# Kernel optimization log

Measured on AMD Instinct MI355X. Metric: run time of the kernel, lower is better.

Reference implementation:

```python
import jax, jax.numpy as jnp
import numpy as np

# static config (matches init_kwargs and a standard 4-level FPN for ~800px input)
SPATIAL_SHAPES = ((100, 100), (50, 50), (25, 25), (13, 13))  # (H_l, W_l)
B, C, H, L, P = 2, 256, 8, 4, 4
DFFN = 2048
DH = C // H
LQ = sum(h * w for h, w in SPATIAL_SHAPES)  # 13294


def layer_norm(x, g, b, eps=1e-5):
    m = jnp.mean(x, -1, keepdims=True)
    v = jnp.mean((x - m) ** 2, -1, keepdims=True)
    return (x - m) * jax.lax.rsqrt(v + eps) * g + b


def ms_deform_sample(value, loc, attn):
    # value [B,Lv,H,DH], loc [B,Lq,H,L,P,2] in [0,1], attn [B,Lq,H,L,P]
    value = jnp.transpose(value, (0, 2, 1, 3))  # [B,H,Lv,DH]
    lq = loc.shape[1]
    out = jnp.zeros((B, H, lq, DH), value.dtype)
    start = 0
    for l, (Hl, Wl) in enumerate(SPATIAL_SHAPES):
        v = jax.lax.dynamic_slice_in_dim(value, start, Hl * Wl, axis=2)  # [B,H,N_l,DH]
        # grid_sample(align_corners=False) coords: x = loc_x*W - 0.5
        gx = jnp.transpose(loc[:, :, :, l, :, 0], (0, 2, 1, 3)) * Wl - 0.5  # [B,H,Lq,P]
        gy = jnp.transpose(loc[:, :, :, l, :, 1], (0, 2, 1, 3)) * Hl - 0.5
        aw = jnp.transpose(attn[:, :, :, l, :], (0, 2, 1, 3))  # [B,H,Lq,P]
        x0 = jnp.floor(gx)
        y0 = jnp.floor(gy)
        for dx in (0.0, 1.0):
            for dy in (0.0, 1.0):
                xi = x0 + dx
                yi = y0 + dy
                w = (1.0 - jnp.abs(gx - xi)) * (1.0 - jnp.abs(gy - yi))
                valid = (xi >= 0) & (xi < Wl) & (yi >= 0) & (yi < Hl)
                idx = (jnp.clip(yi, 0, Hl - 1) * Wl + jnp.clip(xi, 0, Wl - 1)).astype(jnp.int32)
                g = jnp.take_along_axis(v, idx.reshape(B, H, -1)[..., None], axis=2)  # [B,H,Lq*P,DH]
                ww = (w * aw * valid.astype(w.dtype))[..., None]  # [B,H,Lq,P,1]
                out = out + jnp.sum(g.reshape(B, H, lq, P, DH) * ww, axis=3)
        start += Hl * Wl
    return jnp.transpose(out, (0, 2, 1, 3)).reshape(B, lq, C)


def setup_inputs() -> dict:
    key = jax.random.key(0)
    ks = jax.random.split(key, 16)
    s = 0.02
    return {
        "src": jax.random.normal(ks[0], (B, LQ, C), jnp.float32),
        "pos": jax.random.normal(ks[1], (B, LQ, C), jnp.float32),
        "reference_points": jax.random.uniform(ks[2], (B, LQ, L, 2), jnp.float32),
        "w_value": jax.random.normal(ks[3], (C, C), jnp.float32) * s,
        "b_value": jnp.zeros((C,), jnp.float32),
        "w_off": jax.random.normal(ks[4], (C, H * L * P * 2), jnp.float32) * s,
        "b_off": jax.random.normal(ks[5], (H * L * P * 2,), jnp.float32) * s,
        "w_attn": jax.random.normal(ks[6], (C, H * L * P), jnp.float32) * s,
        "b_attn": jnp.zeros((H * L * P,), jnp.float32),
        "w_out": jax.random.normal(ks[7], (C, C), jnp.float32) * s,
        "b_out": jnp.zeros((C,), jnp.float32),
        "ln1_g": jnp.ones((C,), jnp.float32),
        "ln1_b": jnp.zeros((C,), jnp.float32),
        "w_ffn1": jax.random.normal(ks[8], (C, DFFN), jnp.float32) * s,
        "b_ffn1": jnp.zeros((DFFN,), jnp.float32),
        "w_ffn2": jax.random.normal(ks[9], (DFFN, C), jnp.float32) * s,
        "b_ffn2": jnp.zeros((C,), jnp.float32),
        "ln2_g": jnp.ones((C,), jnp.float32),
        "ln2_b": jnp.zeros((C,), jnp.float32),
    }


def reference(src, pos, reference_points, w_value, b_value, w_off, b_off, w_attn, b_attn,
              w_out, b_out, ln1_g, ln1_b, w_ffn1, b_ffn1, w_ffn2, b_ffn2, ln2_g, ln2_b):
    # DeformableTransformerEncoderLayer.forward (eval mode, no dropout)
    q = src + pos  # with_pos_embed
    lq = q.shape[1]
    value = (src @ w_value + b_value).reshape(B, -1, H, DH)
    off = (q @ w_off + b_off).reshape(B, lq, H, L, P, 2)
    attn = (q @ w_attn + b_attn).reshape(B, lq, H, L * P)
    attn = jax.nn.softmax(attn, axis=-1).reshape(B, lq, H, L, P)
    # offset_normalizer = (W_l, H_l)
    norm = jnp.array([[w, h] for h, w in SPATIAL_SHAPES], dtype=src.dtype)
    loc = reference_points[:, :, None, :, None, :] + off / norm[None, None, None, :, None, :]
    src2 = ms_deform_sample(value, loc, attn) @ w_out + b_out
    x = layer_norm(src + src2, ln1_g, ln1_b)
    ff = jax.nn.relu(x @ w_ffn1 + b_ffn1) @ w_ffn2 + b_ffn2
    return layer_norm(x + ff, ln2_g, ln2_b)
```

## Files before the change

kernel.cpp:

```cpp
#include <hip/hip_runtime.h>

#define LQN   13294
#define NBAT  2
#define MROWS (NBAT * LQN)
#define CCH   256
#define NHEAD 8
#define DHEAD 32
#define NLVL  4
#define NPT   4
#define DFF   2048

typedef short short8 __attribute__((ext_vector_type(8)));
typedef float f32x4 __attribute__((ext_vector_type(4)));
typedef unsigned short u16;
typedef u16 u16x4 __attribute__((ext_vector_type(4)));

__device__ __forceinline__ u16 f2bf(float f) {
  unsigned int u = __builtin_bit_cast(unsigned int, f);
  u += 0x7fffu + ((u >> 16) & 1u);
  return (u16)(u >> 16);
}
__device__ __forceinline__ float bf2f(u16 s) {
  unsigned int u = ((unsigned int)s) << 16;
  return __builtin_bit_cast(float, u);
}
__device__ __forceinline__ void async16(const void* g, void* l) {
  __builtin_amdgcn_global_load_lds(
      (const __attribute__((address_space(1))) void*)g,
      (__attribute__((address_space(3))) void*)l, 16, 0, 0);
}

template<int OUT_MODE>
__global__ __launch_bounds__(256, 2)
void gemm_bf16(const u16* __restrict__ A, const u16* __restrict__ BT,
               const float* __restrict__ bias, void* __restrict__ Cout,
               int M, int N, int K)
{
  __shared__ u16 As[2][128 * 64];
  __shared__ u16 Bs[2][128 * 64];
  const int t    = threadIdx.x;
  const int lane = t & 63;
  const int wid  = t >> 6;
  const int wm   = wid >> 1, wn = wid & 1;
  const int bm   = blockIdx.x, bn = blockIdx.y;
  const int l15  = lane & 15;
  const int kq   = lane >> 4;

  f32x4 acc[4][4];
#pragma unroll
  for (int m = 0; m < 4; ++m)
#pragma unroll
    for (int n = 0; n < 4; ++n) acc[m][n] = (f32x4)0.0f;

  auto stage = [&](int buf, int kt) {
#pragma unroll
    for (int i = 0; i < 4; ++i) {
      const int c   = i * 256 + t;
      const int row = c >> 3;
      const int kg  = (c & 7) ^ (row & 7);
      int ar = bm * 128 + row; ar = ar < M ? ar : M - 1;
      async16(&A[(size_t)ar * K + kt + kg * 8], &As[buf][c * 8]);
      const int br = bn * 128 + row;
      async16(&BT[(size_t)br * K + kt + kg * 8], &Bs[buf][c * 8]);
    }
  };

  stage(0, 0);
  __syncthreads();
  int cur = 0;

  for (int kt = 0; kt < K; kt += 64) {
    if (kt + 64 < K) stage(cur ^ 1, kt + 64);

#pragma unroll
    for (int kk = 0; kk < 2; ++kk) {
      short8 af[4], bfr[4];
#pragma unroll
      for (int m = 0; m < 4; ++m) {
        const int row = wm * 64 + m * 16 + l15;
        const int xb  = (kk * 64 + kq * 16) ^ ((row & 7) << 4);
        af[m] = *(const short8*)((const char*)&As[cur][0] + row * 128 + xb);
      }
#pragma unroll
      for (int n = 0; n < 4; ++n) {
        const int col = wn * 64 + n * 16 + l15;
        const int xb  = (kk * 64 + kq * 16) ^ ((col & 7) << 4);
        bfr[n] = *(const short8*)((const char*)&Bs[cur][0] + col * 128 + xb);
      }
#pragma unroll
      for (int m = 0; m < 4; ++m)
#pragma unroll
        for (int n = 0; n < 4; ++n)
          acc[m][n] = __builtin_amdgcn_mfma_f32_16x16x32_bf16(af[m], bfr[n], acc[m][n], 0, 0, 0);
    }

    __syncthreads();
    cur ^= 1;
  }

  const int crow0 = bm * 128 + wm * 64;
  const int ccol0 = bn * 128 + wn * 64;
#pragma unroll
  for (int n = 0; n < 4; ++n) {
    int col = ccol0 + n * 16 + l15;
    float bv = bias[col];
#pragma unroll
    for (int m = 0; m < 4; ++m) {
      int rbase = crow0 + m * 16 + kq * 4;
#pragma unroll
      for (int j = 0; j < 4; ++j) {
        int row = rbase + j;
        if (row < M) {
          float v = acc[m][n][j] + bv;
          if constexpr (OUT_MODE == 0) {
            ((float*)Cout)[(size_t)row * N + col] = v;
          } else {
            if constexpr (OUT_MODE == 2) v = fmaxf(v, 0.0f);
            ((u16*)Cout)[(size_t)row * N + col] = f2bf(v);
          }
        }
      }
    }
  }
}

__global__ __launch_bounds__(512, 2)
void ffn_fused(const u16* __restrict__ x_bf, const u16* __restrict__ W1T,
               const u16* __restrict__ W2T, const float* __restrict__ b1,
               const float* __restrict__ b2, float* __restrict__ out)
{
  extern __shared__ char smem[];
  u16* w1s = (u16*)(smem);
  u16* w2s = (u16*)(smem + 65536);
  char* ps = (char*)(smem + 131072);

  const int t    = threadIdx.x;
  const int lane = t & 63;
  const int wid  = t >> 6;
  const int l15  = lane & 15;
  const int kq   = lane >> 4;
  const int bm   = blockIdx.x;
  const int pwm  = wid >> 1, pwn = wid & 1;
  const int wm   = wid >> 2, wn = wid & 3;

  short8 xr[2][8];
#pragma unroll
  for (int m = 0; m < 2; ++m) {
    int ar = bm * 128 + pwm * 32 + m * 16 + l15;
    ar = ar < MROWS ? ar : MROWS - 1;
    const char* xb = (const char*)x_bf + (size_t)ar * 512 + kq * 16;
#pragma unroll
    for (int ks = 0; ks < 8; ++ks)
      xr[m][ks] = *(const short8*)(xb + ks * 64);
  }

  auto stage = [&](int buf, int it) {
#pragma unroll
    for (int i = 0; i < 4; ++i) {
      const int c  = i * 512 + t;
      const int r1 = c >> 5;
      const int k1 = ((c & 31) ^ (r1 & 7)) * 8;
      async16(&W1T[(size_t)(it * 64 + r1) * 256 + k1], &w1s[buf * 16384 + c * 8]);
      const int r2 = c >> 3;
      const int k2 = ((c & 7) ^ (r2 & 7)) * 8;
      async16(&W2T[(size_t)r2 * 2048 + it * 64 + k2], &w2s[buf * 16384 + c * 8]);
    }
  };

  f32x4 acc[4][4];
#pragma unroll
  for (int m = 0; m < 4; ++m)
#pragma unroll
    for (int n = 0; n < 4; ++n) acc[m][n] = (f32x4)0.0f;

  stage(0, 0);
  __syncthreads();

  for (int it = 0; it < 32; ++it) {
    const int cur = it & 1;
    if (it < 31) stage(cur ^ 1, it + 1);

    f32x4 p[2][2];
#pragma unroll
    for (int m = 0; m < 2; ++m)
#pragma unroll
      for (int n = 0; n < 2; ++n) p[m][n] = (f32x4)0.0f;

#pragma unroll
    for (int ks = 0; ks < 8; ++ks) {
      short8 bfr[2];
#pragma unroll
      for (int n = 0; n < 2; ++n) {
        const int wrow = pwn * 32 + n * 16 + l15;
        const int xb   = (ks * 64 + kq * 16) ^ ((wrow & 7) << 4);
        bfr[n] = *(const short8*)((const char*)&w1s[cur * 16384] + wrow * 512 + xb);
      }
#pragma unroll
      for (int m = 0; m < 2; ++m)
#pragma unroll
        for (int n = 0; n < 2; ++n)
          p[m][n] = __builtin_amdgcn_mfma_f32_16x16x32_bf16(xr[m][ks], bfr[n], p[m][n], 0, 0, 0);
    }

#pragma unroll
    for (int n = 0; n < 2; ++n) {
      const int col = pwn * 32 + n * 16 + l15;
      const float bv = b1[it * 64 + col];
      const int chnk = col >> 3;
      const int sub  = (col & 7) * 2;
#pragma unroll
      for (int m = 0; m < 2; ++m)
#pragma unroll
        for (int j = 0; j < 4; ++j) {
          const int prow = pwm * 32 + m * 16 + kq * 4 + j;
          const float v = fmaxf(p[m][n][j] + bv, 0.0f);
          *(u16*)(ps + prow * 160 + ((chnk ^ ((prow >> 2) & 3)) << 4) + sub) = f2bf(v);
        }
    }
    __syncthreads();

#pragma unroll
    for (int kk = 0; kk < 2; ++kk) {
      short8 paf[4], bfr[4];
#pragma unroll
      for (int m = 0; m < 4; ++m) {
        const int arow = wm * 64 + m * 16 + l15;
        const int c    = kk * 4 + kq;
        paf[m] = *(const short8*)(ps + arow * 160 + ((c ^ ((arow >> 2) & 3)) << 4));
      }
#pragma unroll
      for (int n = 0; n < 4; ++n) {
        const int brow = wn * 64 + n * 16 + l15;
        const int xb   = ((kk * 4 + kq) ^ (brow & 7)) * 16;
        bfr[n] = *(const short8*)((const char*)&w2s[cur * 16384] + brow * 128 + xb);
      }
#pragma unroll
      for (int m = 0; m < 4; ++m)
#pragma unroll
        for (int n = 0; n < 4; ++n)
          acc[m][n] = __builtin_amdgcn_mfma_f32_16x16x32_bf16(paf[m], bfr[n], acc[m][n], 0, 0, 0);
    }
    __syncthreads();
  }

  const int crow0 = bm * 128 + wm * 64;
#pragma unroll
  for (int n = 0; n < 4; ++n) {
    const int col = wn * 64 + n * 16 + l15;
    const float bv = b2[col];
#pragma unroll
    for (int m = 0; m < 4; ++m) {
      const int rbase = crow0 + m * 16 + kq * 4;
#pragma unroll
      for (int j = 0; j < 4; ++j) {
        const int row = rbase + j;
        if (row < MROWS) out[(size_t)row * 256 + col] = acc[m][n][j] + bv;
      }
    }
  }
}

__global__ __launch_bounds__(256)
void sampler_kernel(const float* __restrict__ offattn,
                    const float* __restrict__ refp,
                    const u16*  __restrict__ value,
                    u16*        __restrict__ src2)
{
  __shared__ float2 sWI[2][8][65];

  const int t   = threadIdx.x;
  const int r2  = t >> 7;
  const int g   = t & 127;
  const int row = blockIdx.x * 2 + r2;
  const int b   = row / LQN;

  {
    const int h   = g >> 4;
    const int p16 = g & 15;
    const int l   = p16 >> 2;

    const float* oa = offattn + (size_t)row * 384;

    float logit = oa[256 + h * 16 + p16];
    float mx = logit;
#pragma unroll
    for (int o = 1; o < 16; o <<= 1) mx = fmaxf(mx, __shfl_xor(mx, o, 64));
    float e = __expf(logit - mx);
    float s = e;
#pragma unroll
    for (int o = 1; o < 16; o <<= 1) s += __shfl_xor(s, o, 64);
    const float aw = e / s;

    const int Wl = (l == 0) ? 100 : (l == 1) ? 50 : (l == 2) ? 25 : 13;
    const int Hl = Wl;
    const int st = (l == 0) ? 0 : (l == 1) ? 10000 : (l == 2) ? 12500 : 13125;

    const float ox = oa[(h * 16 + p16) * 2 + 0];
    const float oy = oa[(h * 16 + p16) * 2 + 1];
    const float rx = refp[(size_t)row * 8 + l * 2 + 0] * (float)Wl - 0.5f;
    const float ry = refp[(size_t)row * 8 + l * 2 + 1] * (float)Hl - 0.5f;
    const float gx = rx + ox;
    const float gy = ry + oy;
    const float x0f = floorf(gx), y0f = floorf(gy);
    const int   x0 = (int)x0f, y0 = (int)y0f;
    const float fx = gx - x0f, fy = gy - y0f;

#pragma unroll
    for (int c = 0; c < 4; ++c) {
      const int dx = c & 1, dy = c >> 1;
      const int xi = x0 + dx, yi = y0 + dy;
      const float wx = dx ? fx : 1.0f - fx;
      const float wy = dy ? fy : 1.0f - fy;
      const bool valid = (xi >= 0) && (xi < Wl) && (yi >= 0) && (yi < Hl);
      const int xc = min(max(xi, 0), Wl - 1);
      const int yc = min(max(yi, 0), Hl - 1);
      const int idx = st + yc * Wl + xc;
      const float w = wx * wy * aw * (valid ? 1.0f : 0.0f);
      sWI[r2][h][p16 * 4 + c] = make_float2(w, __builtin_bit_cast(float, idx));
    }
  }
  __syncthreads();

  {
    const int h  = g >> 4;
    const int c2 = g & 15;
    const char* vbase = (const char*)value + (size_t)b * LQN * 512 + h * 64 + c2 * 4;
    const float2* wi = sWI[r2][h];

    float acc0 = 0.f, acc1 = 0.f;
#pragma unroll 16
    for (int e = 0; e < 64; ++e) {
      const float2 p = wi[e];
      const float w  = p.x;
      const int  idx = __builtin_bit_cast(int, p.y);
      const unsigned u = *(const unsigned*)(vbase + (size_t)idx * 512);
      const float f0 = __builtin_bit_cast(float, u << 16);
      const float f1 = __builtin_bit_cast(float, u & 0xffff0000u);
      acc0 += f0 * w;
      acc1 += f1 * w;
    }
    const unsigned o = (unsigned)f2bf(acc0) | ((unsigned)f2bf(acc1) << 16);
    *(unsigned*)&src2[(size_t)row * 256 + h * 32 + c2 * 2] = o;
  }
}

template<int WRITE_BF>
__global__ __launch_bounds__(256)
void ln_kernel(const float* __restrict__ Xa, const float* __restrict__ Xb,
               const float* __restrict__ gam, const float* __restrict__ bet,
               float* __restrict__ Yf, u16* __restrict__ Ybf)
{
  const int wid = threadIdx.x >> 6, lane = threadIdx.x & 63;
  const int row = blockIdx.x * 4 + wid;
  const f32x4 va = ((const f32x4*)(Xa + (size_t)row * 256))[lane];
  const f32x4 vb = ((const f32x4*)(Xb + (size_t)row * 256))[lane];
  f32x4 v = va + vb;
  float s1 = v[0] + v[1] + v[2] + v[3];
  float s2 = v[0] * v[0] + v[1] * v[1] + v[2] * v[2] + v[3] * v[3];
#pragma unroll
  for (int off = 32; off; off >>= 1) {
    s1 += __shfl_xor(s1, off, 64);
    s2 += __shfl_xor(s2, off, 64);
  }
  const float mean = s1 * (1.0f / 256.0f);
  const float var  = s2 * (1.0f / 256.0f) - mean * mean;
  const float rstd = rsqrtf(var + 1e-5f);
  const f32x4 gv = ((const f32x4*)gam)[lane];
  const f32x4 bv = ((const f32x4*)bet)[lane];
  f32x4 y;
#pragma unroll
  for (int j = 0; j < 4; ++j) y[j] = (v[j] - mean) * rstd * gv[j] + bv[j];
  ((f32x4*)(Yf + (size_t)row * 256))[lane] = y;
  if constexpr (WRITE_BF) {
    u16x4 o;
#pragma unroll
    for (int j = 0; j < 4; ++j) o[j] = f2bf(y[j]);
    ((u16x4*)(Ybf + (size_t)row * 256))[lane] = o;
  }
}

__global__ __launch_bounds__(256)
void prep_qsrc(const float* __restrict__ src, const float* __restrict__ pos,
               u16* __restrict__ src_bf, u16* __restrict__ q_bf)
{
  const size_t i = (size_t)blockIdx.x * 256 + threadIdx.x;
  const f32x4 s = ((const f32x4*)src)[i];
  const f32x4 p = ((const f32x4*)pos)[i];
  u16x4 sb, qb;
#pragma unroll
  for (int j = 0; j < 4; ++j) { sb[j] = f2bf(s[j]); qb[j] = f2bf(s[j] + p[j]); }
  ((u16x4*)src_bf)[i] = sb;
  ((u16x4*)q_bf)[i]   = qb;
}

__global__ __launch_bounds__(256)
void transpose_cast(const float* __restrict__ W, u16* __restrict__ WT, int K, int N)
{
  const int i = blockIdx.x * 256 + threadIdx.x;
  if (i >= K * N) return;
  const int k = i / N, n = i - k * N;
  WT[(size_t)n * K + k] = f2bf(W[i]);
}

__global__ __launch_bounds__(256)
void concat_bias(const float* __restrict__ b_off, const float* __restrict__ b_attn,
                 float* __restrict__ out)
{
  const int i = blockIdx.x * 256 + threadIdx.x;
  if (i < 256) out[i] = b_off[i];
  else if (i < 384) out[i] = b_attn[i - 256];
}

extern "C" void kernel_launch(void* const* d_in, const int* in_sizes, int n_in,
                              void* d_out, int out_size, void* d_ws, size_t ws_size,
                              hipStream_t stream)
{
  const float* src     = (const float*)d_in[0];
  const float* pos     = (const float*)d_in[1];
  const float* refp    = (const float*)d_in[2];
  const float* w_value = (const float*)d_in[3];
  const float* b_value = (const float*)d_in[4];
  const float* w_off   = (const float*)d_in[5];
  const float* b_off   = (const float*)d_in[6];
  const float* w_attn  = (const float*)d_in[7];
  const float* b_attn  = (const float*)d_in[8];
  const float* w_out   = (const float*)d_in[9];
  const float* b_out   = (const float*)d_in[10];
  const float* ln1_g   = (const float*)d_in[11];
  const float* ln1_b   = (const float*)d_in[12];
  const float* w_ffn1  = (const float*)d_in[13];
  const float* b_ffn1  = (const float*)d_in[14];
  const float* w_ffn2  = (const float*)d_in[15];
  const float* b_ffn2  = (const float*)d_in[16];
  const float* ln2_g   = (const float*)d_in[17];
  const float* ln2_b   = (const float*)d_in[18];

  char* ws = (char*)d_ws;
  size_t off = 0;
  auto alloc = [&](size_t bytes) { void* p = ws + off; off += (bytes + 255) & ~(size_t)255; return p; };

  u16*   src_bf   = (u16*)  alloc((size_t)MROWS * 256 * 2);
  u16*   q_bf     = (u16*)  alloc((size_t)MROWS * 256 * 2);
  float* offattn  = (float*)alloc((size_t)MROWS * 384 * 4);
  u16*   value_bf = (u16*)  alloc((size_t)MROWS * 256 * 2);
  u16*   src2_bf  = (u16*)  alloc((size_t)MROWS * 256 * 2);
  float* x_f32    = (float*)alloc((size_t)MROWS * 256 * 4);
  u16*   WT_val   = (u16*)  alloc(256 * 256 * 2);
  u16*   WT_oa    = (u16*)  alloc(384 * 256 * 2);
  u16*   WT_out   = (u16*)  alloc(256 * 256 * 2);
  u16*   WT_f1    = (u16*)  alloc(2048 * 256 * 2);
  u16*   WT_f2    = (u16*)  alloc((size_t)256 * 2048 * 2);
  float* bias_oa  = (float*)alloc(384 * 4);

  float* src2p = offattn;
  u16*   x_bf  = q_bf;
  float* ff    = (float*)value_bf;

  transpose_cast<<<256, 256, 0, stream>>>(w_value, WT_val, 256, 256);
  transpose_cast<<<256, 256, 0, stream>>>(w_off, WT_oa, 256, 256);
  transpose_cast<<<128, 256, 0, stream>>>(w_attn, WT_oa + 256 * 256, 256, 128);
  transpose_cast<<<256, 256, 0, stream>>>(w_out, WT_out, 256, 256);
  transpose_cast<<<2048, 256, 0, stream>>>(w_ffn1, WT_f1, 256, 2048);
  transpose_cast<<<2048, 256, 0, stream>>>(w_ffn2, WT_f2, 2048, 256);
  concat_bias<<<2, 256, 0, stream>>>(b_off, b_attn, bias_oa);

  prep_qsrc<<<6647, 256, 0, stream>>>(src, pos, src_bf, q_bf);

  gemm_bf16<1><<<dim3(208, 2), 256, 0, stream>>>(src_bf, WT_val, b_value, value_bf, MROWS, 256, 256);
  gemm_bf16<0><<<dim3(208, 3), 256, 0, stream>>>(q_bf, WT_oa, bias_oa, offattn, MROWS, 384, 256);

  sampler_kernel<<<MROWS / 2, 256, 0, stream>>>(offattn, refp, value_bf, src2_bf);

  gemm_bf16<0><<<dim3(208, 2), 256, 0, stream>>>(src2_bf, WT_out, b_out, src2p, MROWS, 256, 256);

  ln_kernel<1><<<6647, 256, 0, stream>>>(src, src2p, ln1_g, ln1_b, x_f32, x_bf);

  static bool attr_set = false;
  if (!attr_set) {
    hipFuncSetAttribute((const void*)ffn_fused,
                        hipFuncAttributeMaxDynamicSharedMemorySize, 151552);
    attr_set = true;
  }
  ffn_fused<<<208, 512, 151552, stream>>>(x_bf, WT_f1, WT_f2, b_ffn1, b_ffn2, ff);

  ln_kernel<0><<<6647, 256, 0, stream>>>(x_f32, ff, ln2_g, ln2_b, (float*)d_out, nullptr);
}
```

Before: 252.3 us.

## Merge weight prep and value/offset GEMMs into single launches; widen sampler loads

```diff
diff --git a/kernel.cpp b/kernel.cpp
--- a/kernel.cpp
+++ b/kernel.cpp
@@ -112,12 +112,105 @@
         int row = rbase + j;
         if (row < M) {
           float v = acc[m][n][j] + bv;
-          if constexpr (OUT_MODE == 0) {
-            ((float*)Cout)[(size_t)row * N + col] = v;
-          } else {
-            if constexpr (OUT_MODE == 2) v = fmaxf(v, 0.0f);
-            ((u16*)Cout)[(size_t)row * N + col] = f2bf(v);
-          }
+          if constexpr (OUT_MODE == 0) ((float*)Cout)[(size_t)row * N + col] = v;
+          else                         ((u16*)Cout)[(size_t)row * N + col] = f2bf(v);
+        }
+      }
+    }
+  }
+}
+
+__global__ __launch_bounds__(256, 2)
+void gemm_dual(const u16* __restrict__ A0, const u16* __restrict__ BT0,
+               const float* __restrict__ bias0, u16* __restrict__ C0,
+               const u16* __restrict__ A1, const u16* __restrict__ BT1,
+               const float* __restrict__ bias1, float* __restrict__ C1)
+{
+  __shared__ u16 As[2][128 * 64];
+  __shared__ u16 Bs[2][128 * 64];
+  const int t    = threadIdx.x;
+  const int lane = t & 63;
+  const int wid  = t >> 6;
+  const int wm   = wid >> 1, wn = wid & 1;
+  const int bm   = blockIdx.x;
+  const int bnG  = blockIdx.y;
+  const bool first = bnG < 2;
+  const u16* A    = first ? A0 : A1;
+  const u16* BT   = first ? BT0 : BT1;
+  const float* bias = first ? bias0 : bias1;
+  const int  N    = first ? 256 : 384;
+  const int  bn   = first ? bnG : bnG - 2;
+  const int l15  = lane & 15;
+  const int kq   = lane >> 4;
+
+  f32x4 acc[4][4];
+#pragma unroll
+  for (int m = 0; m < 4; ++m)
+#pragma unroll
+    for (int n = 0; n < 4; ++n) acc[m][n] = (f32x4)0.0f;
+
+  auto stage = [&](int buf, int kt) {
+#pragma unroll
+    for (int i = 0; i < 4; ++i) {
+      const int c   = i * 256 + t;
+      const int row = c >> 3;
+      const int kg  = (c & 7) ^ (row & 7);
+      int ar = bm * 128 + row; ar = ar < MROWS ? ar : MROWS - 1;
+      async16(&A[(size_t)ar * 256 + kt + kg * 8], &As[buf][c * 8]);
+      const int br = bn * 128 + row;
+      async16(&BT[(size_t)br * 256 + kt + kg * 8], &Bs[buf][c * 8]);
+    }
+  };
+
+  stage(0, 0);
+  __syncthreads();
+  int cur = 0;
+
+  for (int kt = 0; kt < 256; kt += 64) {
+    if (kt + 64 < 256) stage(cur ^ 1, kt + 64);
+
+#pragma unroll
+    for (int kk = 0; kk < 2; ++kk) {
+      short8 af[4], bfr[4];
+#pragma unroll
+      for (int m = 0; m < 4; ++m) {
+        const int row = wm * 64 + m * 16 + l15;
+        const int xb  = (kk * 64 + kq * 16) ^ ((row & 7) << 4);
+        af[m] = *(const short8*)((const char*)&As[cur][0] + row * 128 + xb);
+      }
+#pragma unroll
+      for (int n = 0; n < 4; ++n) {
+        const int col = wn * 64 + n * 16 + l15;
+        const int xb  = (kk * 64 + kq * 16) ^ ((col & 7) << 4);
+        bfr[n] = *(const short8*)((const char*)&Bs[cur][0] + col * 128 + xb);
+      }
+#pragma unroll
+      for (int m = 0; m < 4; ++m)
+#pragma unroll
+        for (int n = 0; n < 4; ++n)
+          acc[m][n] = __builtin_amdgcn_mfma_f32_16x16x32_bf16(af[m], bfr[n], acc[m][n], 0, 0, 0);
+    }
+
+    __syncthreads();
+    cur ^= 1;
+  }
+
+  const int crow0 = bm * 128 + wm * 64;
+  const int ccol0 = bn * 128 + wn * 64;
+#pragma unroll
+  for (int n = 0; n < 4; ++n) {
+    int col = ccol0 + n * 16 + l15;
+    float bv = bias[col];
+#pragma unroll
+    for (int m = 0; m < 4; ++m) {
+      int rbase = crow0 + m * 16 + kq * 4;
+#pragma unroll
+      for (int j = 0; j < 4; ++j) {
+        int row = rbase + j;
+        if (row < MROWS) {
+          float v = acc[m][n][j] + bv;
+          if (first) C0[(size_t)row * 256 + col] = f2bf(v);
+          else       C1[(size_t)row * 384 + col] = v;
         }
       }
     }
@@ -266,81 +359,82 @@
                     const u16*  __restrict__ value,
                     u16*        __restrict__ src2)
 {
-  __shared__ float2 sWI[2][8][65];
-
-  const int t   = threadIdx.x;
-  const int r2  = t >> 7;
-  const int g   = t & 127;
-  const int row = blockIdx.x * 2 + r2;
-  const int b   = row / LQN;
+  __shared__ float2 sWI[4][8][65];
+
+  const int t    = threadIdx.x;
+  const int r4   = t >> 6;
+  const int lane = t & 63;
+  const int row  = blockIdx.x * 4 + r4;
+  const int b    = row / LQN;
 
   {
-    const int h   = g >> 4;
-    const int p16 = g & 15;
+    const float* oa = offattn + (size_t)row * 384;
+    const float* rp = refp + (size_t)row * 8;
+    const int p16 = lane & 15;
     const int l   = p16 >> 2;
-
-    const float* oa = offattn + (size_t)row * 384;
-
-    float logit = oa[256 + h * 16 + p16];
-    float mx = logit;
-#pragma unroll
-    for (int o = 1; o < 16; o <<= 1) mx = fmaxf(mx, __shfl_xor(mx, o, 64));
-    float e = __expf(logit - mx);
-    float s = e;
-#pragma unroll
-    for (int o = 1; o < 16; o <<= 1) s += __shfl_xor(s, o, 64);
-    const float aw = e / s;
-
-    const int Wl = (l == 0) ? 100 : (l == 1) ? 50 : (l == 2) ? 25 : 13;
-    const int Hl = Wl;
-    const int st = (l == 0) ? 0 : (l == 1) ? 10000 : (l == 2) ? 12500 : 13125;
-
-    const float ox = oa[(h * 16 + p16) * 2 + 0];
-    const float oy = oa[(h * 16 + p16) * 2 + 1];
-    const float rx = refp[(size_t)row * 8 + l * 2 + 0] * (float)Wl - 0.5f;
-    const float ry = refp[(size_t)row * 8 + l * 2 + 1] * (float)Hl - 0.5f;
-    const float gx = rx + ox;
-    const float gy = ry + oy;
-    const float x0f = floorf(gx), y0f = floorf(gy);
-    const int   x0 = (int)x0f, y0 = (int)y0f;
-    const float fx = gx - x0f, fy = gy - y0f;
-
-#pragma unroll
-    for (int c = 0; c < 4; ++c) {
-      const int dx = c & 1, dy = c >> 1;
-      const int xi = x0 + dx, yi = y0 + dy;
-      const float wx = dx ? fx : 1.0f - fx;
-      const float wy = dy ? fy : 1.0f - fy;
-      const bool valid = (xi >= 0) && (xi < Wl) && (yi >= 0) && (yi < Hl);
-      const int xc = min(max(xi, 0), Wl - 1);
-      const int yc = min(max(yi, 0), Hl - 1);
-      const int idx = st + yc * Wl + xc;
-      const float w = wx * wy * aw * (valid ? 1.0f : 0.0f);
-      sWI[r2][h][p16 * 4 + c] = make_float2(w, __builtin_bit_cast(float, idx));
+    const int Wl  = (l == 0) ? 100 : (l == 1) ? 50 : (l == 2) ? 25 : 13;
+    const int st  = (l == 0) ? 0 : (l == 1) ? 10000 : (l == 2) ? 12500 : 13125;
+    const float rx = rp[l * 2 + 0] * (float)Wl - 0.5f;
+    const float ry = rp[l * 2 + 1] * (float)Wl - 0.5f;
+
+#pragma unroll
+    for (int s = 0; s < 2; ++s) {
+      const int h = s * 4 + (lane >> 4);
+      float logit = oa[256 + h * 16 + p16];
+      float mx = logit;
+#pragma unroll
+      for (int o = 1; o < 16; o <<= 1) mx = fmaxf(mx, __shfl_xor(mx, o, 64));
+      float e = __expf(logit - mx);
+      float ssum = e;
+#pragma unroll
+      for (int o = 1; o < 16; o <<= 1) ssum += __shfl_xor(ssum, o, 64);
+      const float aw = e / ssum;
+
+      const float ox = oa[(h * 16 + p16) * 2 + 0];
+      const float oy = oa[(h * 16 + p16) * 2 + 1];
+      const float gx = rx + ox;
+      const float gy = ry + oy;
+      const float x0f = floorf(gx), y0f = floorf(gy);
+      const int   x0 = (int)x0f, y0 = (int)y0f;
+      const float fx = gx - x0f, fy = gy - y0f;
+#pragma unroll
+      for (int c = 0; c < 4; ++c) {
+        const int dx = c & 1, dy = c >> 1;
+        const int xi = x0 + dx, yi = y0 + dy;
+        const float wx = dx ? fx : 1.0f - fx;
+        const float wy = dy ? fy : 1.0f - fy;
+        const bool valid = (xi >= 0) && (xi < Wl) && (yi >= 0) && (yi < Wl);
+        const int xc = min(max(xi, 0), Wl - 1);
+        const int yc = min(max(yi, 0), Wl - 1);
+        const int idx = st + yc * Wl + xc;
+        const float w = wx * wy * aw * (valid ? 1.0f : 0.0f);
+        sWI[r4][h][p16 * 4 + c] = make_float2(w, __builtin_bit_cast(float, idx));
+      }
     }
   }
   __syncthreads();
 
   {
-    const int h  = g >> 4;
-    const int c2 = g & 15;
-    const char* vbase = (const char*)value + (size_t)b * LQN * 512 + h * 64 + c2 * 4;
-    const float2* wi = sWI[r2][h];
-
-    float acc0 = 0.f, acc1 = 0.f;
+    const int h  = lane >> 3;
+    const int c4 = lane & 7;
+    const char* vbase = (const char*)value + (size_t)b * LQN * 512 + h * 64 + c4 * 8;
+    const float2* wi = sWI[r4][h];
+
+    float a0 = 0.f, a1 = 0.f, a2 = 0.f, a3 = 0.f;
 #pragma unroll 16
     for (int e = 0; e < 64; ++e) {
       const float2 p = wi[e];
       const float w  = p.x;
       const int  idx = __builtin_bit_cast(int, p.y);
-      const unsigned u = *(const unsigned*)(vbase + (size_t)idx * 512);
-      const float f0 = __builtin_bit_cast(float, u << 16);
-      const float f1 = __builtin_bit_cast(float, u & 0xffff0000u);
-      acc0 += f0 * w;
-      acc1 += f1 * w;
-    }
-    const unsigned o = (unsigned)f2bf(acc0) | ((unsigned)f2bf(acc1) << 16);
-    *(unsigned*)&src2[(size_t)row * 256 + h * 32 + c2 * 2] = o;
+      const unsigned long long u = *(const unsigned long long*)(vbase + (size_t)idx * 512);
+      a0 += w * bf2f((u16)(u));
+      a1 += w * bf2f((u16)(u >> 16));
+      a2 += w * bf2f((u16)(u >> 32));
+      a3 += w * bf2f((u16)(u >> 48));
+    }
+    u16x4 o;
+    o[0] = f2bf(a0); o[1] = f2bf(a1); o[2] = f2bf(a2); o[3] = f2bf(a3);
+    *(u16x4*)&src2[(size_t)row * 256 + h * 32 + c4 * 4] = o;
   }
 }
 
@@ -394,21 +488,35 @@
 }
 
 __global__ __launch_bounds__(256)
-void transpose_cast(const float* __restrict__ W, u16* __restrict__ WT, int K, int N)
-{
-  const int i = blockIdx.x * 256 + threadIdx.x;
-  if (i >= K * N) return;
-  const int k = i / N, n = i - k * N;
-  WT[(size_t)n * K + k] = f2bf(W[i]);
-}
-
-__global__ __launch_bounds__(256)
-void concat_bias(const float* __restrict__ b_off, const float* __restrict__ b_attn,
-                 float* __restrict__ out)
-{
-  const int i = blockIdx.x * 256 + threadIdx.x;
-  if (i < 256) out[i] = b_off[i];
-  else if (i < 384) out[i] = b_attn[i - 256];
+void prep_weights(const float* __restrict__ w_value, const float* __restrict__ w_off,
+                  const float* __restrict__ w_attn,  const float* __restrict__ w_out,
+                  const float* __restrict__ w_ffn1,  const float* __restrict__ w_ffn2,
+                  const float* __restrict__ b_off,   const float* __restrict__ b_attn,
+                  u16* __restrict__ WT_val, u16* __restrict__ WT_oa, u16* __restrict__ WT_out,
+                  u16* __restrict__ WT_f1,  u16* __restrict__ WT_f2, float* __restrict__ bias_oa)
+{
+  int i = blockIdx.x * 256 + threadIdx.x;
+  if (i < 65536) {
+    const int k = i >> 8, n = i & 255;
+    WT_val[n * 256 + k] = f2bf(w_value[i]);
+  } else if ((i -= 65536) < 65536) {
+    const int k = i >> 8, n = i & 255;
+    WT_oa[n * 256 + k] = f2bf(w_off[i]);
+  } else if ((i -= 65536) < 32768) {
+    const int k = i >> 7, n = i & 127;
+    WT_oa[(256 + n) * 256 + k] = f2bf(w_attn[i]);
+  } else if ((i -= 32768) < 65536) {
+    const int k = i >> 8, n = i & 255;
+    WT_out[n * 256 + k] = f2bf(w_out[i]);
+  } else if ((i -= 65536) < 524288) {
+    const int k = i >> 11, n = i & 2047;
+    WT_f1[n * 256 + k] = f2bf(w_ffn1[i]);
+  } else if ((i -= 524288) < 524288) {
+    const int k = i >> 8, n = i & 255;
+    WT_f2[n * 2048 + k] = f2bf(w_ffn2[i]);
+  } else if ((i -= 524288) < 384) {
+    bias_oa[i] = (i < 256) ? b_off[i] : b_attn[i - 256];
+  }
 }
 
 extern "C" void kernel_launch(void* const* d_in, const int* in_sizes, int n_in,
@@ -456,24 +564,11 @@
   u16*   x_bf  = q_bf;
   float* ff    = (float*)value_bf;
 
-  transpose_cast<<<256, 256, 0, stream>>>(w_value, WT_val, 256, 256);
-  transpose_cast<<<256, 256, 0, stream>>>(w_off, WT_oa, 256, 256);
-  transpose_cast<<<128, 256, 0, stream>>>(w_attn, WT_oa + 256 * 256, 256, 128);
-  transpose_cast<<<256, 256, 0, stream>>>(w_out, WT_out, 256, 256);
-  transpose_cast<<<2048, 256, 0, stream>>>(w_ffn1, WT_f1, 256, 2048);
-  transpose_cast<<<2048, 256, 0, stream>>>(w_ffn2, WT_f2, 2048, 256);
-  concat_bias<<<2, 256, 0, stream>>>(b_off, b_attn, bias_oa);
+  prep_weights<<<4994, 256, 0, stream>>>(w_value, w_off, w_attn, w_out, w_ffn1, w_ffn2,
+                                         b_off, b_attn,
+                                         WT_val, WT_oa, WT_out, WT_f1, WT_f2, bias_oa);
 
   prep_qsrc<<<6647, 256, 0, stream>>>(src, pos, src_bf, q_bf);
-
-  gemm_bf16<1><<<dim3(208, 2), 256, 0, stream>>>(src_bf, WT_val, b_value, value_bf, MROWS, 256, 256);
-  gemm_bf16<0><<<dim3(208, 3), 256, 0, stream>>>(q_bf, WT_oa, bias_oa, offattn, MROWS, 384, 256);
-
-  sampler_kernel<<<MROWS / 2, 256, 0, stream>>>(offattn, refp, value_bf, src2_bf);
-
-  gemm_bf16<0><<<dim3(208, 2), 256, 0, stream>>>(src2_bf, WT_out, b_out, src2p, MROWS, 256, 256);
-
-  ln_kernel<1><<<6647, 256, 0, stream>>>(src, src2p, ln1_g, ln1_b, x_f32, x_bf);
 
   static bool attr_set = false;
   if (!attr_set) {
@@ -481,6 +576,16 @@
                         hipFuncAttributeMaxDynamicSharedMemorySize, 151552);
     attr_set = true;
   }
+
+  gemm_dual<<<dim3(208, 5), 256, 0, stream>>>(src_bf, WT_val, b_value, value_bf,
+                                              q_bf, WT_oa, bias_oa, offattn);
+
+  sampler_kernel<<<MROWS / 4, 256, 0, stream>>>(offattn, refp, value_bf, src2_bf);
+
+  gemm_bf16<0><<<dim3(208, 2), 256, 0, stream>>>(src2_bf, WT_out, b_out, src2p, MROWS, 256, 256);
+
+  ln_kernel<1><<<6647, 256, 0, stream>>>(src, src2p, ln1_g, ln1_b, x_f32, x_bf);
+
   ffn_fused<<<208, 512, 151552, stream>>>(x_bf, WT_f1, WT_f2, b_ffn1, b_ffn2, ff);
 
   ln_kernel<0><<<6647, 256, 0, stream>>>(x_f32, ff, ln2_g, ln2_b, (float*)d_out, nullptr);
```

Measured after the change: 246.4 us. 2.3% less time.
